# Performance work log

Measured on AMD Instinct MI355X. Metric: run time of the kernel, lower is better.

The kernel has to match this reference:

```python
import jax, jax.numpy as jnp
import numpy as np

H = 16          # num_heads
NB = 32         # pos_bias_num_buckets
EPS = 1e-8      # RMSNorm eps


def setup_inputs() -> dict:
    key = jax.random.key(0)
    ks = jax.random.split(key, 8)
    B, L, K, R, M, Dm, Dq = 2, 32, 2, 64, 128, 2048, 2048
    x = jax.random.normal(ks[0], (B, L, K, R, Dm), jnp.float32)
    past_ca_hidden_states = jax.random.normal(ks[1], (B, L, M, Dm), jnp.float32)
    past_ca_attention_mask = jax.random.bernoulli(ks[2], 0.95, (B, L, M)).astype(jnp.float32)
    ln_scale = jnp.ones((Dm,), jnp.float32)
    q_w = jax.random.normal(ks[3], (Dq, Dm), jnp.float32) * 0.02      # torch Linear weight [out,in]
    kv_w = jax.random.normal(ks[4], (2 * Dq, Dm), jnp.float32) * 0.02
    out_w = jax.random.normal(ks[5], (Dm, Dq), jnp.float32) * 0.02
    bias_table = jax.random.normal(ks[6], (NB, H), jnp.float32) * 0.02  # relative_attention_bias.weight
    return dict(x=x, past_ca_hidden_states=past_ca_hidden_states,
                past_ca_attention_mask=past_ca_attention_mask,
                ln_scale=ln_scale, q_w=q_w, kv_w=kv_w, out_w=out_w,
                bias_table=bias_table)


def _rel_bias(bias_table, r, m):
    # linear bucketing, bidirectional=True (RelativePositionBias._relative_position_bucket_linear)
    mn = -(NB // 2) - (NB % 2 - 1)   # -15 for NB=32
    mx = NB // 2                      # 16
    rel = jnp.arange(m)[None, :] - jnp.arange(r)[:, None]   # memory - query, [r, m]
    buckets = jnp.clip(rel, mn, mx) - mn                    # in [0, NB)
    return jnp.transpose(bias_table[buckets], (2, 0, 1))    # [H, r, m]


def reference(x, past_ca_hidden_states, past_ca_attention_mask,
              ln_scale, q_w, kv_w, out_w, bias_table):
    B, L, K, R, Dm = x.shape
    M = past_ca_hidden_states.shape[2]
    Dq = q_w.shape[0]
    dh = Dq // H

    # RMSNorm (p=-1: full norm)
    rms = jnp.linalg.norm(x, axis=-1, keepdims=True) * (Dm ** -0.5)
    xn = (x / (rms + EPS)) * ln_scale

    # projections (no bias)
    q = jnp.einsum('blkrc,qc->blkrq', xn, q_w)                 # [B,L,K,R,Dq]
    kv = jnp.einsum('blmc,qc->blmq', past_ca_hidden_states, kv_w)  # [B,L,M,2Dq]
    k = kv[..., :Dq]
    v = kv[..., Dq:]

    # split heads
    q = q.reshape(B, L, K, R, H, dh).transpose(0, 1, 2, 4, 3, 5)  # [B,L,K,H,R,dh]
    k = k.reshape(B, L, M, H, dh).transpose(0, 1, 3, 2, 4)        # [B,L,H,M,dh]
    v = v.reshape(B, L, M, H, dh).transpose(0, 1, 3, 2, 4)        # [B,L,H,M,dh]

    # NOTE: original applies NO 1/sqrt(dh) scaling
    scores = jnp.einsum('blkhrd,blhmd->blkhrm', q, k)             # [B,L,K,H,R,M]
    scores = scores + _rel_bias(bias_table, R, M)                 # broadcast [H,R,M]
    mask_add = (1.0 - past_ca_attention_mask) * -10000.0          # [B,L,M]
    scores = scores + mask_add[:, :, None, None, None, :]

    attn = jax.nn.softmax(scores, axis=-1)
    out = jnp.einsum('blkhrm,blhmd->blkhrd', attn, v)             # [B,L,K,H,R,dh]
    out = out.transpose(0, 1, 2, 4, 3, 5).reshape(B, L, K, R, Dq)  # merge heads '(h d)'
    out = jnp.einsum('blkrq,cq->blkrc', out, out_w)                # final_proj
    return out + x, attn
```

## Files before the change

### kernel.cpp

```cpp
#include <hip/hip_runtime.h>

typedef _Float16 f16;
typedef _Float16 f16x8 __attribute__((ext_vector_type(8)));
typedef float f32x4 __attribute__((ext_vector_type(4)));

#define LDS_GL16(g, l) __builtin_amdgcn_global_load_lds( \
    (const __attribute__((address_space(1))) void*)(g),  \
    (__attribute__((address_space(3))) void*)(l), 16, 0, 0)
#define VMCNT(N) asm volatile("s_waitcnt vmcnt(" #N ")" ::: "memory")
#define BAR() __builtin_amdgcn_s_barrier()

__global__ __launch_bounds__(256) void prep_kern(
        const float* __restrict__ qw,   f16* __restrict__ qwh,
        const float* __restrict__ kvw,  f16* __restrict__ kvwh,
        const float* __restrict__ outw, f16* __restrict__ outwh,
        const float* __restrict__ hid,  f16* __restrict__ hidh,
        const float* __restrict__ x, const float* __restrict__ lnsc,
        f16* __restrict__ xnh) {
    int b = blockIdx.x;
    if (b >= 16384) {
        long base = (long)(b - 16384) * 2048 + threadIdx.x * 8;
        float4 a = *(const float4*)(x + base);
        float4 v = *(const float4*)(x + base + 4);
        float ss = a.x*a.x + a.y*a.y + a.z*a.z + a.w*a.w
                 + v.x*v.x + v.y*v.y + v.z*v.z + v.w*v.w;
        #pragma unroll
        for (int d = 1; d < 64; d <<= 1) ss += __shfl_xor(ss, d, 64);
        __shared__ float red[4];
        if ((threadIdx.x & 63) == 0) red[threadIdx.x >> 6] = ss;
        __syncthreads();
        ss = red[0] + red[1] + red[2] + red[3];
        float inv = 1.0f / (sqrtf(ss * (1.0f / 2048.0f)) + 1e-8f);
        int c = threadIdx.x * 8;
        float4 s1 = *(const float4*)(lnsc + c);
        float4 s2 = *(const float4*)(lnsc + c + 4);
        f16x8 o = { (f16)(a.x*inv*s1.x),(f16)(a.y*inv*s1.y),(f16)(a.z*inv*s1.z),(f16)(a.w*inv*s1.w),
                    (f16)(v.x*inv*s2.x),(f16)(v.y*inv*s2.y),(f16)(v.z*inv*s2.z),(f16)(v.w*inv*s2.w) };
        *(f16x8*)(xnh + base) = o;
        return;
    }
    const float* in; f16* out; long base;
    if (b < 2048)       { in = qw;   out = qwh;   base = (long)b * 2048; }
    else if (b < 6144)  { in = kvw;  out = kvwh;  base = (long)(b - 2048) * 2048; }
    else if (b < 8192)  { in = outw; out = outwh; base = (long)(b - 6144) * 2048; }
    else                { in = hid;  out = hidh;  base = (long)(b - 8192) * 2048; }
    long o = base + threadIdx.x * 8;
    float4 a = *(const float4*)(in + o);
    float4 c = *(const float4*)(in + o + 4);
    f16x8 v = { (f16)a.x,(f16)a.y,(f16)a.z,(f16)a.w,
                (f16)c.x,(f16)c.y,(f16)c.z,(f16)c.w };
    *(f16x8*)(out + o) = v;
}

template<int EPI>
__device__ __forceinline__ void gemm256_body(
        const f16* __restrict__ A, const f16* __restrict__ B,
        f16* __restrict__ Ch, float* __restrict__ Cf,
        const float* __restrict__ resid, int N, int Kd, int m0, int n0) {
    alignas(16) __shared__ f16 lds[65536];
    int tid = threadIdx.x, lane = tid & 63;
    int wid = tid >> 6, wm = wid >> 2, wn = wid & 3;
    int lr = lane & 15, g = lane >> 4;
    int iL = tid >> 3, cb = tid & 7;

    long goff[8]; int doff[8];
    #pragma unroll
    for (int rd = 0; rd < 2; ++rd) {
        int rA0 = iL + rd * 128;
        goff[0 + rd] = (long)(m0 + rA0) * Kd + ((cb ^ (rA0 & 7)) << 3);
        doff[0 + rd] = rA0 * 64 + cb * 8;
        int rB0 = (iL & 31) + ((iL >> 5) + rd * 2) * 64;
        goff[2 + rd] = (long)(n0 + rB0) * Kd + ((cb ^ (rB0 & 7)) << 3);
        doff[2 + rd] = 32768 + rB0 * 64 + cb * 8;
        int rB1 = rB0 + 32;
        goff[4 + rd] = (long)(n0 + rB1) * Kd + ((cb ^ (rB1 & 7)) << 3);
        doff[4 + rd] = 32768 + rB1 * 64 + cb * 8;
        int rA1 = rA0 + 64;
        goff[6 + rd] = (long)(m0 + rA1) * Kd + ((cb ^ (rA1 & 7)) << 3);
        doff[6 + rd] = rA1 * 64 + cb * 8;
    }
    auto stage = [&](int kt, int p, int r) {
        const f16* src = (r == 0 || r == 3) ? A : B;
        #pragma unroll
        for (int rd = 0; rd < 2; ++rd)
            LDS_GL16(src + goff[r * 2 + rd] + kt * 64,
                     lds + p * 16384 + doff[r * 2 + rd]);
    };

    const char* ldsc = (const char*)lds;
    int swz = lr & 7;
    const char* baseA[2], *baseB[2];
    baseA[0] = ldsc + (wm * 128 + lr) * 128 + ((g ^ swz) << 4);
    baseA[1] = ldsc + (wm * 128 + lr) * 128 + (((4 + g) ^ swz) << 4);
    baseB[0] = ldsc + 65536 + (wn * 64 + lr) * 128 + ((g ^ swz) << 4);
    baseB[1] = ldsc + 65536 + (wn * 64 + lr) * 128 + (((4 + g) ^ swz) << 4);

    f32x4 acc[8][4] = {};
    f16x8 a[4][2], b0[2][2], b1[2][2];

    auto loadA = [&](int bufB, int qm) {
        #pragma unroll
        for (int mf = 0; mf < 4; ++mf)
            #pragma unroll
            for (int kk = 0; kk < 2; ++kk)
                a[mf][kk] = *(const f16x8*)(baseA[kk] + bufB + qm * 8192 + mf * 2048);
    };
    auto loadB = [&](f16x8 (&d)[2][2], int bufB, int qn) {
        #pragma unroll
        for (int nf = 0; nf < 2; ++nf)
            #pragma unroll
            for (int kk = 0; kk < 2; ++kk)
                d[nf][kk] = *(const f16x8*)(baseB[kk] + bufB + qn * 4096 + nf * 2048);
    };
    auto mma = [&](f16x8 (&bb)[2][2], int qm, int qn) {
        __builtin_amdgcn_s_setprio(1);
        #pragma unroll
        for (int kk = 0; kk < 2; ++kk)
            #pragma unroll
            for (int mf = 0; mf < 4; ++mf)
                #pragma unroll
                for (int nf = 0; nf < 2; ++nf)
                    acc[qm * 4 + mf][qn * 2 + nf] = __builtin_amdgcn_mfma_f32_16x16x32_f16(
                        a[mf][kk], bb[nf][kk], acc[qm * 4 + mf][qn * 2 + nf], 0, 0, 0);
        __builtin_amdgcn_s_setprio(0);
    };

    int NT = Kd >> 6, NI = NT >> 1;

    stage(0, 0, 0); stage(0, 0, 1); stage(0, 0, 2); stage(0, 0, 3);
    stage(1, 1, 0); stage(1, 1, 1); stage(1, 1, 2);
    VMCNT(6); BAR();

    for (int it = 0; it < NI - 1; ++it) {
        int t0 = it * 2;
        loadA(0, 0); loadB(b0, 0, 0);
        stage(t0 + 1, 1, 3);
        BAR(); mma(b0, 0, 0); BAR();
        loadB(b1, 0, 1);
        stage(t0 + 2, 0, 0);
        BAR(); mma(b1, 0, 1); BAR();
        loadA(0, 1);
        stage(t0 + 2, 0, 1);
        BAR(); mma(b1, 1, 1); BAR();
        stage(t0 + 2, 0, 2);
        VMCNT(6);
        BAR(); mma(b0, 1, 0); BAR();
        loadA(32768, 0); loadB(b0, 32768, 0);
        stage(t0 + 2, 0, 3);
        BAR(); mma(b0, 0, 0); BAR();
        loadB(b1, 32768, 1);
        stage(t0 + 3, 1, 0);
        BAR(); mma(b1, 0, 1); BAR();
        loadA(32768, 1);
        stage(t0 + 3, 1, 1);
        BAR(); mma(b1, 1, 1); BAR();
        stage(t0 + 3, 1, 2);
        VMCNT(6);
        BAR(); mma(b0, 1, 0); BAR();
    }
    {
        loadA(0, 0); loadB(b0, 0, 0);
        stage(NT - 1, 1, 3);
        BAR(); mma(b0, 0, 0); BAR();
        loadB(b1, 0, 1);
        BAR(); mma(b1, 0, 1); BAR();
        loadA(0, 1);
        BAR(); mma(b1, 1, 1); BAR();
        VMCNT(0);
        BAR(); mma(b0, 1, 0); BAR();
        loadA(32768, 0); loadB(b0, 32768, 0);
        BAR(); mma(b0, 0, 0); BAR();
        loadB(b1, 32768, 1);
        BAR(); mma(b1, 0, 1); BAR();
        loadA(32768, 1);
        BAR(); mma(b1, 1, 1); BAR();
        BAR(); mma(b0, 1, 0);
    }

    __syncthreads();
    if (EPI == 0) {
        #pragma unroll
        for (int i = 0; i < 8; ++i)
            #pragma unroll
            for (int j = 0; j < 4; ++j)
                #pragma unroll
                for (int reg = 0; reg < 4; ++reg) {
                    int row = wm * 128 + i * 16 + g * 4 + reg;
                    int col = (wn * 64 + j * 16 + lr) ^ ((row & 12) << 2);
                    lds[row * 256 + col] = (f16)acc[i][j][reg];
                }
        __syncthreads();
        #pragma unroll
        for (int k = 0; k < 16; ++k) {
            int e = k * 4096 + tid * 8;
            int row = e >> 8, col = e & 255;
            *(f16x8*)(Ch + (long)(m0 + row) * N + n0 + col) =
                *(const f16x8*)(lds + row * 256 + (col ^ ((row & 12) << 2)));
        }
    } else {
        float* Ct = (float*)lds;
        #pragma unroll
        for (int h = 0; h < 2; ++h) {
            if (h) __syncthreads();
            if (wm == h) {
                #pragma unroll
                for (int i = 0; i < 8; ++i)
                    #pragma unroll
                    for (int j = 0; j < 4; ++j)
                        #pragma unroll
                        for (int reg = 0; reg < 4; ++reg) {
                            int row = i * 16 + g * 4 + reg;
                            int col = (wn * 64 + j * 16 + lr) ^ ((row & 4) << 2);
                            Ct[row * 256 + col] = acc[i][j][reg];
                        }
            }
            __syncthreads();
            #pragma unroll
            for (int k = 0; k < 8; ++k) {
                int e = k * 4096 + tid * 8;
                int row = e >> 8, col = e & 255;
                int pc = col ^ ((row & 4) << 2);
                long gi = (long)(m0 + h * 128 + row) * N + n0 + col;
                float4 c0 = *(const float4*)(Ct + row * 256 + pc);
                float4 c1 = *(const float4*)(Ct + row * 256 + pc + 4);
                float4 r0 = *(const float4*)(resid + gi);
                float4 r1 = *(const float4*)(resid + gi + 4);
                c0.x += r0.x; c0.y += r0.y; c0.z += r0.z; c0.w += r0.w;
                c1.x += r1.x; c1.y += r1.y; c1.z += r1.z; c1.w += r1.w;
                *(float4*)(Cf + gi) = c0;
                *(float4*)(Cf + gi + 4) = c1;
            }
        }
    }
}

__global__ __launch_bounds__(512, 2) void gemm_qkv(
        const f16* __restrict__ Aq, const f16* __restrict__ Bq, f16* __restrict__ Cq,
        const f16* __restrict__ Akv, const f16* __restrict__ Bkv, f16* __restrict__ Ckv) {
    int fid = (blockIdx.x & 7) * 96 + (blockIdx.x >> 3);
    const f16 *A, *B; f16* C; int N, lf, sh;
    if (fid < 256) { A = Aq;  B = Bq;  C = Cq;  N = 2048; lf = fid;       sh = 3; }
    else           { A = Akv; B = Bkv; C = Ckv; N = 4096; lf = fid - 256; sh = 4; }
    int by = lf >> sh, bx = lf & ((1 << sh) - 1);
    gemm256_body<0>(A, B, C, nullptr, nullptr, N, 2048, by << 8, bx << 8);
}

__global__ __launch_bounds__(512, 2) void gemm_out(
        const f16* __restrict__ A, const f16* __restrict__ B,
        float* __restrict__ Cf, const float* __restrict__ resid) {
    int fid = (blockIdx.x & 7) * 32 + (blockIdx.x >> 3);
    int by = fid >> 3, bx = fid & 7;
    gemm256_body<1>(A, B, nullptr, Cf, resid, 2048, 2048, by << 8, bx << 8);
}

__global__ __launch_bounds__(256, 2) void attn_kern(
        const f16* __restrict__ Q,
        const f16* __restrict__ KV,
        const float* __restrict__ mask,
        const float* __restrict__ bias,
        float* __restrict__ attn_out,
        f16* __restrict__ pv_out) {
    __shared__ f16 Vt[128 * 128];
    __shared__ f16 P[64 * 136];
    int blk = blockIdx.x;
    int h  = blk & 15;
    int bk = blk >> 4;
    int bl = bk >> 1;
    int tid = threadIdx.x, lane = tid & 63, w = tid >> 6;
    int r0 = w << 4;
    int lr = lane & 15, g = lane >> 4;
    long qbase  = (long)bk * 64 * 2048;
    long kvbase = (long)bl * 128 * 4096;
    f16x8 vreg[8];
    const f16* vsrc = KV + kvbase + 2048 + h * 128;
    #pragma unroll
    for (int rnd = 0; rnd < 8; ++rnd) {
        int idx = tid + rnd * 256;
        vreg[rnd] = *(const f16x8*)(vsrc + (long)(idx >> 4) * 4096 + (idx & 15) * 8);
    }
    f16x8 aq[4];
    const f16* qrow = Q + qbase + (long)(r0 + lr) * 2048 + h * 128 + g * 8;
    #pragma unroll
    for (int t4 = 0; t4 < 4; ++t4) aq[t4] = *(const f16x8*)(qrow + t4 * 32);
    f32x4 s[8] = {};
    const f16* kbase = KV + kvbase + h * 128 + g * 8;
    #pragma unroll
    for (int j = 0; j < 8; ++j) {
        #pragma unroll
        for (int t4 = 0; t4 < 4; ++t4) {
            f16x8 bkf = *(const f16x8*)(kbase + (long)(j * 16 + lr) * 4096 + t4 * 32);
            s[j] = __builtin_amdgcn_mfma_f32_16x16x32_f16(aq[t4], bkf, s[j], 0, 0, 0);
        }
    }
    float madd[8];
    #pragma unroll
    for (int j = 0; j < 8; ++j)
        madd[j] = (1.0f - mask[(long)bl * 128 + j * 16 + lr]) * -10000.0f;
    #pragma unroll
    for (int reg = 0; reg < 4; ++reg) {
        int r = r0 + g * 4 + reg;
        float mx = -3.0e38f;
        #pragma unroll
        for (int j = 0; j < 8; ++j) {
            int m = j * 16 + lr;
            int rel = m - r;
            int bkt = (rel < -15 ? -15 : (rel > 16 ? 16 : rel)) + 15;
            float v = s[j][reg] + bias[bkt * 16 + h] + madd[j];
            s[j][reg] = v;
            mx = fmaxf(mx, v);
        }
        #pragma unroll
        for (int d = 1; d < 16; d <<= 1) mx = fmaxf(mx, __shfl_xor(mx, d, 64));
        float sum = 0.0f;
        #pragma unroll
        for (int j = 0; j < 8; ++j) {
            float e = __expf(s[j][reg] - mx);
            s[j][reg] = e;
            sum += e;
        }
        #pragma unroll
        for (int d = 1; d < 16; d <<= 1) sum += __shfl_xor(sum, d, 64);
        float inv = 1.0f / sum;
        #pragma unroll
        for (int j = 0; j < 8; ++j) s[j][reg] *= inv;
    }
    long abase = (long)blk * 64 * 128;
    #pragma unroll
    for (int reg = 0; reg < 4; ++reg) {
        int r = r0 + g * 4 + reg;
        #pragma unroll
        for (int j = 0; j < 8; ++j) {
            attn_out[abase + (long)r * 128 + j * 16 + lr] = s[j][reg];
            P[r * 136 + j * 16 + lr] = (f16)s[j][reg];
        }
    }
    {
        char* vtb = (char*)Vt;
        #pragma unroll
        for (int rnd = 0; rnd < 8; ++rnd) {
            int idx = tid + rnd * 256;
            int k = idx >> 4, c0 = (idx & 15) * 8;
            #pragma unroll
            for (int i = 0; i < 8; ++i) {
                int c = c0 + i;
                int sx = ((c >> 3) ^ i) & 7;
                *(f16*)(vtb + c * 256 + ((k * 2) ^ (sx << 4))) = vreg[rnd][i];
            }
        }
    }
    __syncthreads();
    f16x8 pa[4];
    #pragma unroll
    for (int t4 = 0; t4 < 4; ++t4)
        pa[t4] = *(const f16x8*)(P + (r0 + lr) * 136 + t4 * 32 + g * 8);
    f32x4 o[8] = {};
    const char* vtb = (const char*)Vt;
    #pragma unroll
    for (int dj = 0; dj < 8; ++dj) {
        int c = dj * 16 + lr;
        int sc = (((c >> 3) ^ (c & 7)) & 7) << 4;
        const char* vrow = vtb + c * 256;
        #pragma unroll
        for (int t4 = 0; t4 < 4; ++t4) {
            f16x8 bv = *(const f16x8*)(vrow + ((t4 * 64 + g * 16) ^ sc));
            o[dj] = __builtin_amdgcn_mfma_f32_16x16x32_f16(pa[t4], bv, o[dj], 0, 0, 0);
        }
    }
    __syncthreads();
    #pragma unroll
    for (int dj = 0; dj < 8; ++dj)
        #pragma unroll
        for (int reg = 0; reg < 4; ++reg) {
            int row = r0 + g * 4 + reg;
            int col = (dj * 16 + lr) ^ ((row & 12) << 2);
            Vt[row * 128 + col] = (f16)o[dj][reg];
        }
    __syncthreads();
    f16* ob = pv_out + qbase + h * 128;
    #pragma unroll
    for (int k = 0; k < 4; ++k) {
        int e = k * 2048 + tid * 8;
        int row = e >> 7, col = e & 127;
        *(f16x8*)(ob + (long)row * 2048 + col) =
            *(const f16x8*)(Vt + row * 128 + (col ^ ((row & 12) << 2)));
    }
}

extern "C" void kernel_launch(void* const* d_in, const int* in_sizes, int n_in,
                              void* d_out, int out_size, void* d_ws, size_t ws_size,
                              hipStream_t stream) {
    const float* x     = (const float*)d_in[0];
    const float* hid   = (const float*)d_in[1];
    const float* mask  = (const float*)d_in[2];
    const float* lnsc  = (const float*)d_in[3];
    const float* q_w   = (const float*)d_in[4];
    const float* kv_w  = (const float*)d_in[5];
    const float* out_w = (const float*)d_in[6];
    const float* bias  = (const float*)d_in[7];
    float* out0 = (float*)d_out;
    float* attn = out0 + 16777216;

    f16* kv_h  = (f16*)out0;
    f16* xn_h  = (f16*)attn;
    f16* hid_h = (f16*)(attn + 8388608);
    char* ws = (char*)d_ws;
    f16* q_h    = (f16*)(ws);
    f16* ao_h   = (f16*)(ws + 33554432L);
    f16* qw_h   = (f16*)(ws + 67108864L);
    f16* kvw_h  = (f16*)(ws + 75497472L);
    f16* outw_h = (f16*)(ws + 92274688L);

    prep_kern<<<24576, 256, 0, stream>>>(q_w, qw_h, kv_w, kvw_h,
                                         out_w, outw_h, hid, hid_h,
                                         x, lnsc, xn_h);
    gemm_qkv<<<768, 512, 0, stream>>>(xn_h, qw_h, q_h, hid_h, kvw_h, kv_h);
    attn_kern<<<2048, 256, 0, stream>>>(q_h, kv_h, mask, bias, attn, ao_h);
    gemm_out<<<256, 512, 0, stream>>>(ao_h, outw_h, out0, x);
}
```

Measured before the change: 370.1 us.

## Use 4-wave 256x256 GEMM tiles with 128x128 per-wave fragments and register prefetch

Reworks the shared GEMM body from 8 waves (each computing a 128x64 sub-tile) to 4 waves (each computing 128x128), doubling per-wave accumulators. LDS fragments for the next MFMA phase are now loaded into separate register buffers before the current phase runs, and the barrier before each phase is paired with a vmcnt wait. The global-to-LDS staging is remapped so each thread issues four loads per stage, and launch bounds drop to 256 threads with one block per CU. The intent is to cut LDS traffic per FLOP and overlap fragment loads with MFMA, at the cost of higher register pressure and lower occupancy.

```diff
diff --git a/kernel.cpp b/kernel.cpp
--- a/kernel.cpp
+++ b/kernel.cpp
@@ -59,32 +59,28 @@
         const float* __restrict__ resid, int N, int Kd, int m0, int n0) {
     alignas(16) __shared__ f16 lds[65536];
     int tid = threadIdx.x, lane = tid & 63;
-    int wid = tid >> 6, wm = wid >> 2, wn = wid & 3;
+    int wid = tid >> 6, wm = wid >> 1, wn = wid & 1;
     int lr = lane & 15, g = lane >> 4;
-    int iL = tid >> 3, cb = tid & 7;
-
-    long goff[8]; int doff[8];
-    #pragma unroll
-    for (int rd = 0; rd < 2; ++rd) {
-        int rA0 = iL + rd * 128;
-        goff[0 + rd] = (long)(m0 + rA0) * Kd + ((cb ^ (rA0 & 7)) << 3);
-        doff[0 + rd] = rA0 * 64 + cb * 8;
-        int rB0 = (iL & 31) + ((iL >> 5) + rd * 2) * 64;
-        goff[2 + rd] = (long)(n0 + rB0) * Kd + ((cb ^ (rB0 & 7)) << 3);
-        doff[2 + rd] = 32768 + rB0 * 64 + cb * 8;
-        int rB1 = rB0 + 32;
-        goff[4 + rd] = (long)(n0 + rB1) * Kd + ((cb ^ (rB1 & 7)) << 3);
-        doff[4 + rd] = 32768 + rB1 * 64 + cb * 8;
-        int rA1 = rA0 + 64;
-        goff[6 + rd] = (long)(m0 + rA1) * Kd + ((cb ^ (rA1 & 7)) << 3);
-        doff[6 + rd] = rA1 * 64 + cb * 8;
-    }
+
+    long gA[4], gB[4]; int dL[4];
+    #pragma unroll
+    for (int ld = 0; ld < 4; ++ld) {
+        int idx = ld * 256 + tid;
+        int sub = idx >> 3, c8 = idx & 7;
+        int row = (sub & 63) + ((sub >> 6) << 7);
+        gA[ld] = (long)(m0 + row) * Kd + ((c8 ^ (row & 7)) << 3);
+        gB[ld] = (long)(n0 + row) * Kd + ((c8 ^ (row & 7)) << 3);
+        dL[ld] = row * 64 + c8 * 8;
+    }
+    long rowskip = (long)64 * Kd;
     auto stage = [&](int kt, int p, int r) {
-        const f16* src = (r == 0 || r == 3) ? A : B;
-        #pragma unroll
-        for (int rd = 0; rd < 2; ++rd)
-            LDS_GL16(src + goff[r * 2 + rd] + kt * 64,
-                     lds + p * 16384 + doff[r * 2 + rd]);
+        #pragma unroll
+        for (int ld = 0; ld < 4; ++ld) {
+            if (r == 0)      LDS_GL16(A + gA[ld] + kt * 64,           lds + p * 16384 + dL[ld]);
+            else if (r == 3) LDS_GL16(A + gA[ld] + rowskip + kt * 64, lds + p * 16384 + dL[ld] + 4096);
+            else if (r == 1) LDS_GL16(B + gB[ld] + kt * 64,           lds + 32768 + p * 16384 + dL[ld]);
+            else             LDS_GL16(B + gB[ld] + rowskip + kt * 64, lds + 32768 + p * 16384 + dL[ld] + 4096);
+        }
     };
 
     const char* ldsc = (const char*)lds;
@@ -92,36 +88,29 @@
     const char* baseA[2], *baseB[2];
     baseA[0] = ldsc + (wm * 128 + lr) * 128 + ((g ^ swz) << 4);
     baseA[1] = ldsc + (wm * 128 + lr) * 128 + (((4 + g) ^ swz) << 4);
-    baseB[0] = ldsc + 65536 + (wn * 64 + lr) * 128 + ((g ^ swz) << 4);
-    baseB[1] = ldsc + 65536 + (wn * 64 + lr) * 128 + (((4 + g) ^ swz) << 4);
-
-    f32x4 acc[8][4] = {};
-    f16x8 a[4][2], b0[2][2], b1[2][2];
-
-    auto loadA = [&](int bufB, int qm) {
-        #pragma unroll
-        for (int mf = 0; mf < 4; ++mf)
+    baseB[0] = ldsc + 65536 + (wn * 128 + lr) * 128 + ((g ^ swz) << 4);
+    baseB[1] = ldsc + 65536 + (wn * 128 + lr) * 128 + (((4 + g) ^ swz) << 4);
+
+    f32x4 acc[8][8] = {};
+    f16x8 a0f[4][2], a1f[4][2], b0e[4][2], b0o[4][2], b1f[4][2];
+
+    auto loadF = [&](f16x8 (&d)[4][2], const char* const (&bs)[2], int bufB, int q) {
+        #pragma unroll
+        for (int f = 0; f < 4; ++f)
             #pragma unroll
             for (int kk = 0; kk < 2; ++kk)
-                a[mf][kk] = *(const f16x8*)(baseA[kk] + bufB + qm * 8192 + mf * 2048);
+                d[f][kk] = *(const f16x8*)(bs[kk] + bufB + q * 8192 + f * 2048);
     };
-    auto loadB = [&](f16x8 (&d)[2][2], int bufB, int qn) {
-        #pragma unroll
-        for (int nf = 0; nf < 2; ++nf)
-            #pragma unroll
-            for (int kk = 0; kk < 2; ++kk)
-                d[nf][kk] = *(const f16x8*)(baseB[kk] + bufB + qn * 4096 + nf * 2048);
-    };
-    auto mma = [&](f16x8 (&bb)[2][2], int qm, int qn) {
+    auto mma = [&](f16x8 (&aa)[4][2], f16x8 (&bb)[4][2], int qm, int qn) {
         __builtin_amdgcn_s_setprio(1);
         #pragma unroll
         for (int kk = 0; kk < 2; ++kk)
             #pragma unroll
             for (int mf = 0; mf < 4; ++mf)
                 #pragma unroll
-                for (int nf = 0; nf < 2; ++nf)
-                    acc[qm * 4 + mf][qn * 2 + nf] = __builtin_amdgcn_mfma_f32_16x16x32_f16(
-                        a[mf][kk], bb[nf][kk], acc[qm * 4 + mf][qn * 2 + nf], 0, 0, 0);
+                for (int nf = 0; nf < 4; ++nf)
+                    acc[qm * 4 + mf][qn * 4 + nf] = __builtin_amdgcn_mfma_f32_16x16x32_f16(
+                        aa[mf][kk], bb[nf][kk], acc[qm * 4 + mf][qn * 4 + nf], 0, 0, 0);
         __builtin_amdgcn_s_setprio(0);
     };
 
@@ -129,52 +118,67 @@
 
     stage(0, 0, 0); stage(0, 0, 1); stage(0, 0, 2); stage(0, 0, 3);
     stage(1, 1, 0); stage(1, 1, 1); stage(1, 1, 2);
-    VMCNT(6); BAR();
+    VMCNT(12); BAR();
+    loadF(a0f, baseA, 0, 0);
+    loadF(b0e, baseB, 0, 0);
 
     for (int it = 0; it < NI - 1; ++it) {
         int t0 = it * 2;
-        loadA(0, 0); loadB(b0, 0, 0);
+        loadF(b1f, baseB, 0, 1);
         stage(t0 + 1, 1, 3);
-        BAR(); mma(b0, 0, 0); BAR();
-        loadB(b1, 0, 1);
+        VMCNT(16); BAR();
+        mma(a0f, b0e, 0, 0);
+        loadF(a1f, baseA, 0, 1);
         stage(t0 + 2, 0, 0);
-        BAR(); mma(b1, 0, 1); BAR();
-        loadA(0, 1);
+        VMCNT(16); BAR();
+        mma(a0f, b1f, 0, 1);
+        loadF(a0f, baseA, 32768, 0);
         stage(t0 + 2, 0, 1);
-        BAR(); mma(b1, 1, 1); BAR();
+        VMCNT(16); BAR();
+        mma(a1f, b1f, 1, 1);
+        loadF(b0o, baseB, 32768, 0);
         stage(t0 + 2, 0, 2);
-        VMCNT(6);
-        BAR(); mma(b0, 1, 0); BAR();
-        loadA(32768, 0); loadB(b0, 32768, 0);
+        VMCNT(16); BAR();
+        mma(a1f, b0e, 1, 0);
+        loadF(b1f, baseB, 32768, 1);
         stage(t0 + 2, 0, 3);
-        BAR(); mma(b0, 0, 0); BAR();
-        loadB(b1, 32768, 1);
+        VMCNT(16); BAR();
+        mma(a0f, b0o, 0, 0);
+        loadF(a1f, baseA, 32768, 1);
         stage(t0 + 3, 1, 0);
-        BAR(); mma(b1, 0, 1); BAR();
-        loadA(32768, 1);
+        VMCNT(16); BAR();
+        mma(a0f, b1f, 0, 1);
+        loadF(a0f, baseA, 0, 0);
         stage(t0 + 3, 1, 1);
-        BAR(); mma(b1, 1, 1); BAR();
+        VMCNT(16); BAR();
+        mma(a1f, b1f, 1, 1);
+        loadF(b0e, baseB, 0, 0);
         stage(t0 + 3, 1, 2);
-        VMCNT(6);
-        BAR(); mma(b0, 1, 0); BAR();
+        VMCNT(16); BAR();
+        mma(a1f, b0o, 1, 0);
     }
     {
-        loadA(0, 0); loadB(b0, 0, 0);
+        loadF(b1f, baseB, 0, 1);
         stage(NT - 1, 1, 3);
-        BAR(); mma(b0, 0, 0); BAR();
-        loadB(b1, 0, 1);
-        BAR(); mma(b1, 0, 1); BAR();
-        loadA(0, 1);
-        BAR(); mma(b1, 1, 1); BAR();
-        VMCNT(0);
-        BAR(); mma(b0, 1, 0); BAR();
-        loadA(32768, 0); loadB(b0, 32768, 0);
-        BAR(); mma(b0, 0, 0); BAR();
-        loadB(b1, 32768, 1);
-        BAR(); mma(b1, 0, 1); BAR();
-        loadA(32768, 1);
-        BAR(); mma(b1, 1, 1); BAR();
-        BAR(); mma(b0, 1, 0);
+        VMCNT(16); BAR();
+        mma(a0f, b0e, 0, 0);
+        loadF(a1f, baseA, 0, 1);
+        VMCNT(12); BAR();
+        mma(a0f, b1f, 0, 1);
+        loadF(a0f, baseA, 32768, 0);
+        VMCNT(8); BAR();
+        mma(a1f, b1f, 1, 1);
+        loadF(b0o, baseB, 32768, 0);
+        VMCNT(4); BAR();
+        mma(a1f, b0e, 1, 0);
+        loadF(b1f, baseB, 32768, 1);
+        VMCNT(0); BAR();
+        mma(a0f, b0o, 0, 0);
+        loadF(a1f, baseA, 32768, 1);
+        BAR();
+        mma(a0f, b1f, 0, 1);
+        mma(a1f, b1f, 1, 1);
+        mma(a1f, b0o, 1, 0);
     }
 
     __syncthreads();
@@ -182,17 +186,17 @@
         #pragma unroll
         for (int i = 0; i < 8; ++i)
             #pragma unroll
-            for (int j = 0; j < 4; ++j)
+            for (int j = 0; j < 8; ++j)
                 #pragma unroll
                 for (int reg = 0; reg < 4; ++reg) {
                     int row = wm * 128 + i * 16 + g * 4 + reg;
-                    int col = (wn * 64 + j * 16 + lr) ^ ((row & 12) << 2);
+                    int col = (wn * 128 + j * 16 + lr) ^ ((row & 12) << 2);
                     lds[row * 256 + col] = (f16)acc[i][j][reg];
                 }
         __syncthreads();
         #pragma unroll
-        for (int k = 0; k < 16; ++k) {
-            int e = k * 4096 + tid * 8;
+        for (int k = 0; k < 32; ++k) {
+            int e = k * 2048 + tid * 8;
             int row = e >> 8, col = e & 255;
             *(f16x8*)(Ch + (long)(m0 + row) * N + n0 + col) =
                 *(const f16x8*)(lds + row * 256 + (col ^ ((row & 12) << 2)));
@@ -206,18 +210,18 @@
                 #pragma unroll
                 for (int i = 0; i < 8; ++i)
                     #pragma unroll
-                    for (int j = 0; j < 4; ++j)
+                    for (int j = 0; j < 8; ++j)
                         #pragma unroll
                         for (int reg = 0; reg < 4; ++reg) {
                             int row = i * 16 + g * 4 + reg;
-                            int col = (wn * 64 + j * 16 + lr) ^ ((row & 4) << 2);
+                            int col = (wn * 128 + j * 16 + lr) ^ ((row & 4) << 2);
                             Ct[row * 256 + col] = acc[i][j][reg];
                         }
             }
             __syncthreads();
             #pragma unroll
-            for (int k = 0; k < 8; ++k) {
-                int e = k * 4096 + tid * 8;
+            for (int k = 0; k < 16; ++k) {
+                int e = k * 2048 + tid * 8;
                 int row = e >> 8, col = e & 255;
                 int pc = col ^ ((row & 4) << 2);
                 long gi = (long)(m0 + h * 128 + row) * N + n0 + col;
@@ -234,7 +238,7 @@
     }
 }
 
-__global__ __launch_bounds__(512, 2) void gemm_qkv(
+__global__ __launch_bounds__(256, 1) void gemm_qkv(
         const f16* __restrict__ Aq, const f16* __restrict__ Bq, f16* __restrict__ Cq,
         const f16* __restrict__ Akv, const f16* __restrict__ Bkv, f16* __restrict__ Ckv) {
     int fid = (blockIdx.x & 7) * 96 + (blockIdx.x >> 3);
@@ -245,7 +249,7 @@
     gemm256_body<0>(A, B, C, nullptr, nullptr, N, 2048, by << 8, bx << 8);
 }
 
-__global__ __launch_bounds__(512, 2) void gemm_out(
+__global__ __launch_bounds__(256, 1) void gemm_out(
         const f16* __restrict__ A, const f16* __restrict__ B,
         float* __restrict__ Cf, const float* __restrict__ resid) {
     int fid = (blockIdx.x & 7) * 32 + (blockIdx.x >> 3);
@@ -413,7 +417,7 @@
     prep_kern<<<24576, 256, 0, stream>>>(q_w, qw_h, kv_w, kvw_h,
                                          out_w, outw_h, hid, hid_h,
                                          x, lnsc, xn_h);
-    gemm_qkv<<<768, 512, 0, stream>>>(xn_h, qw_h, q_h, hid_h, kvw_h, kv_h);
+    gemm_qkv<<<768, 256, 0, stream>>>(xn_h, qw_h, q_h, hid_h, kvw_h, kv_h);
     attn_kern<<<2048, 256, 0, stream>>>(q_h, kv_h, mask, bias, attn, ao_h);
-    gemm_out<<<256, 512, 0, stream>>>(ao_h, outw_h, out0, x);
-}
+    gemm_out<<<256, 256, 0, stream>>>(ao_h, outw_h, out0, x);
+}
```

Measured after the change: 405.5 us. 1.1x slower.
